# Kernel optimization log

Measured on AMD Instinct MI355X. Metric: run time of the kernel, lower is better.

## Reference

```python
import jax, jax.numpy as jnp
import numpy as np

N = 50000
E = 800000
EPS = 1e-5


def graph_conv(x, src, dst, ew, W_rel, b_rel, W_root):
    # PyG GraphConv (aggr='add'): lin_rel(sum_j e_ij * x_j) + lin_root(x_i)
    msg = x[src] * ew[:, None]                      # [E, F_in]
    agg = jax.ops.segment_sum(msg, dst, num_segments=N)  # [N, F_in]
    return agg @ W_rel.T + b_rel + x @ W_root.T


def batchnorm_relu(h, gamma, beta):
    mu = jnp.mean(h, axis=0)
    var = jnp.mean(jnp.square(h - mu), axis=0)
    hn = (h - mu) * jax.lax.rsqrt(var + EPS)
    return jax.nn.relu(hn * gamma + beta)


def setup_inputs() -> dict:
    key = jax.random.key(0)
    ks = jax.random.split(key, 16)
    d_in, h, d_out = 128, 256, 64

    def lin(k, fo, fi):
        return jax.random.normal(k, (fo, fi), jnp.float32) * (1.0 / np.sqrt(fi))

    return {
        "x": jax.random.normal(ks[0], (N, d_in), jnp.float32),
        "edge_index": jax.random.randint(ks[1], (2, E), 0, N, jnp.int32),
        "edge_weight": jax.random.uniform(ks[2], (E,), jnp.float32),
        "Wr0": lin(ks[3], h, d_in), "br0": jnp.zeros((h,), jnp.float32), "Wt0": lin(ks[4], h, d_in),
        "g0": jnp.ones((h,), jnp.float32), "be0": jnp.zeros((h,), jnp.float32),
        "Wr1": lin(ks[5], h, h), "br1": jnp.zeros((h,), jnp.float32), "Wt1": lin(ks[6], h, h),
        "g1": jnp.ones((h,), jnp.float32), "be1": jnp.zeros((h,), jnp.float32),
        "Wr2": lin(ks[7], d_out, h), "br2": jnp.zeros((d_out,), jnp.float32), "Wt2": lin(ks[8], d_out, h),
    }


def reference(x, edge_index, edge_weight, Wr0, br0, Wt0, g0, be0,
              Wr1, br1, Wt1, g1, be1, Wr2, br2, Wt2):
    src, dst = edge_index[0], edge_index[1]
    h = graph_conv(x, src, dst, edge_weight, Wr0, br0, Wt0)
    h = batchnorm_relu(h, g0, be0)
    h = graph_conv(h, src, dst, edge_weight, Wr1, br1, Wt1)
    h = batchnorm_relu(h, g1, be1)
    return graph_conv(h, src, dst, edge_weight, Wr2, br2, Wt2)
```

## Files before the change

kernel.cpp:

```cpp
#include <hip/hip_runtime.h>
#include <cstddef>
#include <cstdint>

#define SCAN_B 512

using bf16x8 = __attribute__((ext_vector_type(8))) short;
using f32x4  = __attribute__((ext_vector_type(4))) float;

__device__ __forceinline__ unsigned short f2bf(float f) {
    unsigned int u = __builtin_bit_cast(unsigned int, f);
    return (unsigned short)((u + 0x7FFFu + ((u >> 16) & 1u)) >> 16);
}
__device__ __forceinline__ float bf2f(unsigned short b) {
    unsigned int u = ((unsigned int)b) << 16;
    return __builtin_bit_cast(float, u);
}
__device__ __forceinline__ float i2f(int i) { return __builtin_bit_cast(float, i); }
__device__ __forceinline__ float u2f(unsigned int u) { return __builtin_bit_cast(float, u); }
__device__ __forceinline__ void gload_lds16(const void* g, void* l) {
    __builtin_amdgcn_global_load_lds((const __attribute__((address_space(1))) void*)g,
                                     (__attribute__((address_space(3))) void*)l, 16, 0, 0);
}

__global__ void hist_conv_k(const int* __restrict__ dst, int* __restrict__ counts,
                            int* __restrict__ rank, int E, int histBlocks,
                            const float* __restrict__ x, const float* __restrict__ Wr0,
                            const float* __restrict__ Wt0, const float* __restrict__ Wr1,
                            const float* __restrict__ Wt1, const float* __restrict__ Wr2,
                            const float* __restrict__ Wt2, unsigned short* __restrict__ x_bf,
                            unsigned short* __restrict__ Wr0b, unsigned short* __restrict__ Wt0b,
                            unsigned short* __restrict__ Wr1b, unsigned short* __restrict__ Wt1b,
                            unsigned short* __restrict__ Wr2b, unsigned short* __restrict__ Wt2b,
                            int n4x) {
    if ((int)blockIdx.x < histBlocks) {
        int e = blockIdx.x * 256 + threadIdx.x;
        if (e < E) rank[e] = atomicAdd(&counts[dst[e]], 1);
        return;
    }
    int j = (blockIdx.x - histBlocks) * 256 + threadIdx.x;
    const float* s;
    unsigned short* d;
    if (j < n4x) { s = x; d = x_bf; }
    else {
        j -= n4x;
        if (j < 8192) { s = Wr0; d = Wr0b; }
        else { j -= 8192;
        if (j < 8192) { s = Wt0; d = Wt0b; }
        else { j -= 8192;
        if (j < 16384) { s = Wr1; d = Wr1b; }
        else { j -= 16384;
        if (j < 16384) { s = Wt1; d = Wt1b; }
        else { j -= 16384;
        if (j < 4096) { s = Wr2; d = Wr2b; }
        else { j -= 4096;
        if (j >= 4096) return;
        s = Wt2; d = Wt2b; } } } } }
    }
    float4 v = reinterpret_cast<const float4*>(s)[j];
    ushort4 o;
    o.x = f2bf(v.x); o.y = f2bf(v.y); o.z = f2bf(v.z); o.w = f2bf(v.w);
    reinterpret_cast<ushort4*>(d)[j] = o;
}

__global__ void scan1_k(const int* __restrict__ counts, int* __restrict__ partial,
                        int* __restrict__ blocksum, int Nn) {
    __shared__ int sh[SCAN_B];
    int i = blockIdx.x * SCAN_B + threadIdx.x;
    int v = (i < Nn) ? counts[i] : 0;
    sh[threadIdx.x] = v;
    __syncthreads();
    for (int off = 1; off < SCAN_B; off <<= 1) {
        int t = (threadIdx.x >= (unsigned)off) ? sh[threadIdx.x - off] : 0;
        __syncthreads();
        sh[threadIdx.x] += t;
        __syncthreads();
    }
    if (i < Nn) partial[i] = sh[threadIdx.x];
    if (threadIdx.x == SCAN_B - 1) blocksum[blockIdx.x] = sh[threadIdx.x];
}

__global__ void scan3b_k(const int* __restrict__ partial, const int* __restrict__ blocksum,
                         int* __restrict__ offsets, int Nn) {
    __shared__ int add_s;
    int bx = blockIdx.x;
    if (threadIdx.x < 64) {
        int s = 0;
        for (int j = threadIdx.x; j < bx; j += 64) s += blocksum[j];
        #pragma unroll
        for (int off = 32; off > 0; off >>= 1) s += __shfl_down(s, off, 64);
        if (threadIdx.x == 0) add_s = s;
    }
    __syncthreads();
    int i = bx * SCAN_B + threadIdx.x;
    if (i >= Nn) return;
    offsets[i + 1] = partial[i] + add_s;
    if (i == 0) offsets[0] = 0;
}

__global__ void fill2_k(const int* __restrict__ src, const int* __restrict__ dst,
                        const float* __restrict__ ew, const int* __restrict__ offsets,
                        const int* __restrict__ rank, int2* __restrict__ e_sw, int E) {
    int e = blockIdx.x * blockDim.x + threadIdx.x;
    if (e >= E) return;
    int pos = offsets[dst[e]] + rank[e];
    e_sw[pos] = make_int2(src[e], __builtin_bit_cast(int, ew[e]));
}

__global__ void gather128_k(const unsigned short* __restrict__ x, const int* __restrict__ offsets,
                            const int2* __restrict__ e_sw, unsigned short* __restrict__ agg, int Nn) {
    int wid = __builtin_amdgcn_readfirstlane((blockIdx.x * blockDim.x + threadIdx.x) >> 6);
    int lane = threadIdx.x & 63;
    if (wid >= Nn) return;
    int p = offsets[wid], end = offsets[wid + 1];
    const char* xb = (const char*)x;
    const unsigned loff = lane * 4u;
    float a0 = 0.f, a1 = 0.f;
    for (; p + 8 <= end; p += 8) {
        int2 ee[8];
        #pragma unroll
        for (int i = 0; i < 8; ++i) ee[i] = e_sw[p + i];
        unsigned vv[8];
        #pragma unroll
        for (int i = 0; i < 8; ++i)
            vv[i] = *reinterpret_cast<const unsigned*>(xb + ((unsigned)ee[i].x * 256u + loff));
        #pragma unroll
        for (int i = 0; i < 8; ++i) {
            float w = i2f(ee[i].y);
            a0 += w * u2f(vv[i] << 16); a1 += w * u2f(vv[i] & 0xFFFF0000u);
        }
    }
    for (; p < end; ++p) {
        int2 e0 = e_sw[p];
        unsigned v0 = *reinterpret_cast<const unsigned*>(xb + ((unsigned)e0.x * 256u + loff));
        float w = i2f(e0.y);
        a0 += w * u2f(v0 << 16); a1 += w * u2f(v0 & 0xFFFF0000u);
    }
    unsigned o = (unsigned)f2bf(a0) | ((unsigned)f2bf(a1) << 16);
    *reinterpret_cast<unsigned*>(agg + (size_t)wid * 128 + lane * 2) = o;
}

__global__ void gather_bn_k(const unsigned short* __restrict__ h_raw,
                            const float* __restrict__ sums, const float* __restrict__ sumsq,
                            const float* __restrict__ g, const float* __restrict__ be,
                            const int* __restrict__ offsets, const int2* __restrict__ e_sw,
                            unsigned short* __restrict__ agg, unsigned short* __restrict__ hN,
                            float invN, int Nn, int gBlocks) {
    const int lane = threadIdx.x & 63;
    if ((int)blockIdx.x >= gBlocks) {
        int total4 = Nn * 64;
        int stride = (gridDim.x - gBlocks) * 256;
        for (int t = (blockIdx.x - gBlocks) * 256 + threadIdx.x; t < total4; t += stride) {
            int f0 = (t & 63) * 4;
            float4 sm = *reinterpret_cast<const float4*>(sums + f0);
            float4 sq = *reinterpret_cast<const float4*>(sumsq + f0);
            float4 gg = *reinterpret_cast<const float4*>(g + f0);
            float4 bb = *reinterpret_cast<const float4*>(be + f0);
            float smv[4] = {sm.x, sm.y, sm.z, sm.w};
            float sqv[4] = {sq.x, sq.y, sq.z, sq.w};
            float ggv[4] = {gg.x, gg.y, gg.z, gg.w};
            float bbv[4] = {bb.x, bb.y, bb.z, bb.w};
            ushort4 v = reinterpret_cast<const ushort4*>(h_raw)[t];
            unsigned short vv[4] = {v.x, v.y, v.z, v.w};
            ushort4 o;
            unsigned short* op = &o.x;
            #pragma unroll
            for (int c = 0; c < 4; ++c) {
                float mu = smv[c] * invN;
                float var = sqv[c] * invN - mu * mu;
                float sc = ggv[c] * rsqrtf(var + 1e-5f);
                float sh = bbv[c] - mu * sc;
                op[c] = f2bf(fmaxf(bf2f(vv[c]) * sc + sh, 0.f));
            }
            reinterpret_cast<ushort4*>(hN)[t] = o;
        }
        return;
    }
    int wid = __builtin_amdgcn_readfirstlane((blockIdx.x * blockDim.x + threadIdx.x) >> 6);
    if (wid >= Nn) return;
    int f0 = lane * 4;
    float4 sm = *reinterpret_cast<const float4*>(sums + f0);
    float4 sq = *reinterpret_cast<const float4*>(sumsq + f0);
    float4 gg = *reinterpret_cast<const float4*>(g + f0);
    float4 bb = *reinterpret_cast<const float4*>(be + f0);
    float sc0, sc1, sc2, sc3, sh0, sh1, sh2, sh3;
    {
        float mu, var;
        mu = sm.x * invN; var = sq.x * invN - mu * mu; sc0 = gg.x * rsqrtf(var + 1e-5f); sh0 = bb.x - mu * sc0;
        mu = sm.y * invN; var = sq.y * invN - mu * mu; sc1 = gg.y * rsqrtf(var + 1e-5f); sh1 = bb.y - mu * sc1;
        mu = sm.z * invN; var = sq.z * invN - mu * mu; sc2 = gg.z * rsqrtf(var + 1e-5f); sh2 = bb.z - mu * sc2;
        mu = sm.w * invN; var = sq.w * invN - mu * mu; sc3 = gg.w * rsqrtf(var + 1e-5f); sh3 = bb.w - mu * sc3;
    }
    int p = offsets[wid], end = offsets[wid + 1];
    const char* xb = (const char*)h_raw;
    const unsigned loff = lane * 8u;
    float a0 = 0.f, a1 = 0.f, a2 = 0.f, a3 = 0.f;
    for (; p + 8 <= end; p += 8) {
        int2 ee[8];
        #pragma unroll
        for (int i = 0; i < 8; ++i) ee[i] = e_sw[p + i];
        uint2 vv[8];
        #pragma unroll
        for (int i = 0; i < 8; ++i)
            vv[i] = *reinterpret_cast<const uint2*>(xb + ((unsigned)ee[i].x * 512u + loff));
        #pragma unroll
        for (int i = 0; i < 8; ++i) {
            float w = i2f(ee[i].y);
            a0 += w * fmaxf(u2f(vv[i].x << 16) * sc0 + sh0, 0.f);
            a1 += w * fmaxf(u2f(vv[i].x & 0xFFFF0000u) * sc1 + sh1, 0.f);
            a2 += w * fmaxf(u2f(vv[i].y << 16) * sc2 + sh2, 0.f);
            a3 += w * fmaxf(u2f(vv[i].y & 0xFFFF0000u) * sc3 + sh3, 0.f);
        }
    }
    for (; p < end; ++p) {
        int2 e0 = e_sw[p];
        uint2 v0 = *reinterpret_cast<const uint2*>(xb + ((unsigned)e0.x * 512u + loff));
        float w = i2f(e0.y);
        a0 += w * fmaxf(u2f(v0.x << 16) * sc0 + sh0, 0.f);
        a1 += w * fmaxf(u2f(v0.x & 0xFFFF0000u) * sc1 + sh1, 0.f);
        a2 += w * fmaxf(u2f(v0.y << 16) * sc2 + sh2, 0.f);
        a3 += w * fmaxf(u2f(v0.y & 0xFFFF0000u) * sc3 + sh3, 0.f);
    }
    uint2 o;
    o.x = (unsigned)f2bf(a0) | ((unsigned)f2bf(a1) << 16);
    o.y = (unsigned)f2bf(a2) | ((unsigned)f2bf(a3) << 16);
    *reinterpret_cast<uint2*>(agg + (size_t)wid * 256 + lane * 4) = o;
}

__global__ void gather_out_k(const unsigned short* __restrict__ t, const float* __restrict__ root,
                             const int* __restrict__ offsets, const int2* __restrict__ e_sw,
                             float* __restrict__ out, int Nn) {
    int gt = blockIdx.x * blockDim.x + threadIdx.x;
    int node = gt >> 4;
    int li = gt & 15;
    if (node >= Nn) return;
    int p = offsets[node], end = offsets[node + 1];
    const char* tb = (const char*)t;
    const unsigned loff = li * 8u;
    float a0 = 0.f, a1 = 0.f, a2 = 0.f, a3 = 0.f;
    for (; p + 8 <= end; p += 8) {
        int2 ee[8];
        #pragma unroll
        for (int i = 0; i < 8; ++i) ee[i] = e_sw[p + i];
        uint2 vv[8];
        #pragma unroll
        for (int i = 0; i < 8; ++i)
            vv[i] = *reinterpret_cast<const uint2*>(tb + ((unsigned)ee[i].x * 128u + loff));
        #pragma unroll
        for (int i = 0; i < 8; ++i) {
            float w = i2f(ee[i].y);
            a0 += w * u2f(vv[i].x << 16); a1 += w * u2f(vv[i].x & 0xFFFF0000u);
            a2 += w * u2f(vv[i].y << 16); a3 += w * u2f(vv[i].y & 0xFFFF0000u);
        }
    }
    for (; p < end; ++p) {
        int2 e0 = e_sw[p];
        uint2 v0 = *reinterpret_cast<const uint2*>(tb + ((unsigned)e0.x * 128u + loff));
        float w = i2f(e0.y);
        a0 += w * u2f(v0.x << 16); a1 += w * u2f(v0.x & 0xFFFF0000u);
        a2 += w * u2f(v0.y << 16); a3 += w * u2f(v0.y & 0xFFFF0000u);
    }
    float4 r = *reinterpret_cast<const float4*>(root + (size_t)node * 64 + li * 4);
    float4 o = make_float4(r.x + a0, r.y + a1, r.z + a2, r.w + a3);
    *reinterpret_cast<float4*>(out + (size_t)node * 64 + li * 4) = o;
}

template<int K, int O, int MODE>
__global__ __launch_bounds__(512, 4) void gemm_mfma_k(
        const unsigned short* __restrict__ A, const unsigned short* __restrict__ Wa,
        const unsigned short* __restrict__ X, const unsigned short* __restrict__ Wb,
        const float* __restrict__ bias, unsigned short* __restrict__ out_bf,
        float* __restrict__ out_f, float* __restrict__ sums, float* __restrict__ sumsq,
        int Nn) {
    constexpr int BM = 128, BN = 128;
    constexpr int MI = 4;
    constexpr int OJ = 2;
    constexpr int KSTEPS = K / 32;
    constexpr int NT = (MODE == 0 ? 2 : 1) * KSTEPS;
    __shared__ unsigned short As[2][BM * 32];
    __shared__ unsigned short Bs[2][BN * 32];
    const int tid = threadIdx.x;
    const int w = tid >> 6, l = tid & 63;
    const int wr = w >> 2, wc = w & 3;
    const int lrow = l & 15, kgrp = l >> 4;
    int bx = blockIdx.x;
    bx = (bx & 7) * (gridDim.x >> 3) + (bx >> 3);
    const int m0 = bx * BM;
    const int n0 = blockIdx.y * BN;
    const int srow = tid >> 2, sslot = tid & 3;
    const int gslot = sslot ^ ((srow >> 1) & 3);

    auto stage = [&](int buf, int t) {
        int ph = t / KSTEPS;
        int k0 = (t % KSTEPS) * 32;
        const unsigned short* Ap = (MODE == 0 && ph) ? X : A;
        const unsigned short* Wp = (MODE == 0 && ph) ? Wb : Wa;
        gload_lds16(Ap + (size_t)(m0 + srow) * K + k0 + (gslot << 3), &As[buf][w * 512]);
        gload_lds16(Wp + (size_t)(n0 + srow) * K + k0 + (gslot << 3), &Bs[buf][w * 512]);
    };

    f32x4 acc[MI][OJ];
    #pragma unroll
    for (int i = 0; i < MI; ++i)
        #pragma unroll
        for (int j = 0; j < OJ; ++j) {
            f32x4 z = {0.f, 0.f, 0.f, 0.f};
            acc[i][j] = z;
        }

    stage(0, 0);
    __syncthreads();
    #pragma unroll
    for (int t = 0; t < NT; ++t) {
        const int cur = t & 1;
        if (t + 1 < NT) stage(cur ^ 1, t + 1);
        bf16x8 a[MI], b[OJ];
        #pragma unroll
        for (int mi = 0; mi < MI; ++mi) {
            int row = wr * 64 + mi * 16 + lrow;
            int slot = kgrp ^ ((row >> 1) & 3);
            a[mi] = *reinterpret_cast<const bf16x8*>(&As[cur][row * 32 + slot * 8]);
        }
        #pragma unroll
        for (int oj = 0; oj < OJ; ++oj) {
            int row = wc * 32 + oj * 16 + lrow;
            int slot = kgrp ^ ((row >> 1) & 3);
            b[oj] = *reinterpret_cast<const bf16x8*>(&Bs[cur][row * 32 + slot * 8]);
        }
        #pragma unroll
        for (int mi = 0; mi < MI; ++mi)
            #pragma unroll
            for (int oj = 0; oj < OJ; ++oj)
                acc[mi][oj] = __builtin_amdgcn_mfma_f32_16x16x32_bf16(
                    a[mi], b[oj], acc[mi][oj], 0, 0, 0);
        __syncthreads();
    }

    if constexpr (MODE == 0) {
        #pragma unroll
        for (int oj = 0; oj < OJ; ++oj) {
            int col = n0 + wc * 32 + oj * 16 + lrow;
            float bcol = bias[col];
            float s = 0.f, q = 0.f;
            #pragma unroll
            for (int mi = 0; mi < MI; ++mi) {
                #pragma unroll
                for (int r = 0; r < 4; ++r) {
                    int row = m0 + wr * 64 + mi * 16 + kgrp * 4 + r;
                    float v = acc[mi][oj][r] + bcol;
                    if (row < Nn) {
                        out_bf[(size_t)row * O + col] = f2bf(v);
                        s += v; q += v * v;
                    }
                }
            }
            s += __shfl_xor(s, 16, 64); q += __shfl_xor(q, 16, 64);
            s += __shfl_xor(s, 32, 64); q += __shfl_xor(q, 32, 64);
            if (kgrp == 0) {
                atomicAdd(&sums[col], s);
                atomicAdd(&sumsq[col], q);
            }
        }
    } else {
        #pragma unroll
        for (int oj = 0; oj < OJ; ++oj) {
            int col = n0 + wc * 32 + oj * 16 + lrow;
            #pragma unroll
            for (int mi = 0; mi < MI; ++mi) {
                #pragma unroll
                for (int r = 0; r < 4; ++r) {
                    int row = m0 + wr * 64 + mi * 16 + kgrp * 4 + r;
                    if (row < Nn) {
                        if (col < 64)
                            out_bf[(size_t)row * 64 + col] = f2bf(acc[mi][oj][r]);
                        else
                            out_f[(size_t)row * 64 + (col - 64)] = acc[mi][oj][r] + bias[col - 64];
                    }
                }
            }
        }
    }
}

__global__ void bn_relu_bf_k(const unsigned short* __restrict__ h, const float* __restrict__ sums,
                             const float* __restrict__ sumsq, const float* __restrict__ g,
                             const float* __restrict__ be, unsigned short* __restrict__ hb,
                             float invN, int total4) {
    int t = blockIdx.x * blockDim.x + threadIdx.x;
    if (t >= total4) return;
    int f0 = (t & 63) * 4;
    float4 sm = *reinterpret_cast<const float4*>(sums + f0);
    float4 sq = *reinterpret_cast<const float4*>(sumsq + f0);
    float4 gg = *reinterpret_cast<const float4*>(g + f0);
    float4 bb = *reinterpret_cast<const float4*>(be + f0);
    float smv[4] = {sm.x, sm.y, sm.z, sm.w};
    float sqv[4] = {sq.x, sq.y, sq.z, sq.w};
    float ggv[4] = {gg.x, gg.y, gg.z, gg.w};
    float bbv[4] = {bb.x, bb.y, bb.z, bb.w};
    ushort4 v = reinterpret_cast<const ushort4*>(h)[t];
    unsigned short vv[4] = {v.x, v.y, v.z, v.w};
    ushort4 o;
    unsigned short* op = &o.x;
    #pragma unroll
    for (int c = 0; c < 4; ++c) {
        float mu = smv[c] * invN;
        float var = sqv[c] * invN - mu * mu;
        float sc = ggv[c] * rsqrtf(var + 1e-5f);
        float sh = bbv[c] - mu * sc;
        op[c] = f2bf(fmaxf(bf2f(vv[c]) * sc + sh, 0.f));
    }
    reinterpret_cast<ushort4*>(hb)[t] = o;
}

extern "C" void kernel_launch(void* const* d_in, const int* in_sizes, int n_in,
                              void* d_out, int out_size, void* d_ws, size_t ws_size,
                              hipStream_t stream) {
    const float* x   = (const float*)d_in[0];
    const int*   ei  = (const int*)d_in[1];
    const float* ew  = (const float*)d_in[2];
    const float* Wr0 = (const float*)d_in[3];
    const float* br0 = (const float*)d_in[4];
    const float* Wt0 = (const float*)d_in[5];
    const float* g0  = (const float*)d_in[6];
    const float* be0 = (const float*)d_in[7];
    const float* Wr1 = (const float*)d_in[8];
    const float* br1 = (const float*)d_in[9];
    const float* Wt1 = (const float*)d_in[10];
    const float* g1  = (const float*)d_in[11];
    const float* be1 = (const float*)d_in[12];
    const float* Wr2 = (const float*)d_in[13];
    const float* br2 = (const float*)d_in[14];
    const float* Wt2 = (const float*)d_in[15];

    const int E  = in_sizes[2];
    const int Nn = in_sizes[0] / 128;
    const size_t NP = 50176;
    const int* src = ei;
    const int* dst = ei + E;

    unsigned short* x_bf   = (unsigned short*)d_ws;
    unsigned short* agg_bf = x_bf + NP * 128;
    unsigned short* h0N    = agg_bf + NP * 256;
    unsigned short* h1N    = h0N + NP * 256;
    unsigned short* h_bf   = h1N + NP * 256;
    unsigned short* t_bf   = h_bf + NP * 256;
    unsigned short* wbf    = t_bf + NP * 64;
    unsigned short* Wr0b = wbf;
    unsigned short* Wt0b = wbf + 32768;
    unsigned short* Wr1b = wbf + 65536;
    unsigned short* Wt1b = wbf + 131072;
    unsigned short* W2cat = wbf + 196608;
    float* root  = (float*)(wbf + 229376);
    int2*  e_sw  = (int2*)(root + NP * 64);
    float* stats = (float*)(e_sw + E);
    int*   counts  = (int*)(stats + 4096);
    int*   partial = counts + Nn;
    int*   blocksum = partial + Nn;
    int*   rank    = blocksum + 512;
    int*   offsets = rank + E;

    dim3 blk(256);
    const int nbScan = (Nn + SCAN_B - 1) / SCAN_B;
    const float invN = 1.0f / (float)Nn;
    const int n4x = Nn * 32;
    const int histBlocks = (E + 255) / 256;
    const int convBlocks = (n4x + 57344 + 255) / 256;

    hipMemsetAsync(stats, 0, (4096 + (size_t)Nn) * sizeof(float), stream);

    hist_conv_k<<<dim3(histBlocks + convBlocks), blk, 0, stream>>>(
        dst, counts, rank, E, histBlocks,
        x, Wr0, Wt0, Wr1, Wt1, Wr2, Wt2,
        x_bf, Wr0b, Wt0b, Wr1b, Wt1b, W2cat, W2cat + 16384, n4x);
    scan1_k<<<dim3(nbScan), dim3(SCAN_B), 0, stream>>>(counts, partial, blocksum, Nn);
    scan3b_k<<<dim3(nbScan), dim3(SCAN_B), 0, stream>>>(partial, blocksum, offsets, Nn);
    fill2_k<<<dim3(histBlocks), blk, 0, stream>>>(src, dst, ew, offsets, rank, e_sw, E);

    const int gatherBlocks = (Nn * 64 + 255) / 256;

    gather128_k<<<dim3(gatherBlocks), blk, 0, stream>>>(x_bf, offsets, e_sw, agg_bf, Nn);
    gemm_mfma_k<128, 256, 0><<<dim3(NP / 128, 2), dim3(512), 0, stream>>>(
        agg_bf, Wr0b, x_bf, Wt0b, br0, h_bf, nullptr, stats + 0, stats + 256, Nn);

    gather_bn_k<<<dim3(gatherBlocks + 2048), blk, 0, stream>>>(
        h_bf, stats + 0, stats + 256, g0, be0, offsets, e_sw,
        agg_bf, h0N, invN, Nn, gatherBlocks);

    gemm_mfma_k<256, 256, 0><<<dim3(NP / 128, 2), dim3(512), 0, stream>>>(
        agg_bf, Wr1b, h0N, Wt1b, br1, h_bf, nullptr, stats + 1024, stats + 1280, Nn);
    bn_relu_bf_k<<<dim3((Nn * 64 + 255) / 256), blk, 0, stream>>>(
        h_bf, stats + 1024, stats + 1280, g1, be1, h1N, invN, Nn * 64);

    gemm_mfma_k<256, 128, 1><<<dim3(NP / 128, 1), dim3(512), 0, stream>>>(
        h1N, W2cat, nullptr, nullptr, br2, t_bf, root, nullptr, nullptr, Nn);
    gather_out_k<<<dim3((Nn * 16 + 255) / 256), blk, 0, stream>>>(
        t_bf, root, offsets, e_sw, (float*)d_out, Nn);
}
```

Measured before the change: 295.9 us.

## Fuse second BatchNorm+ReLU into final GEMM operand load

Drops the standalone BN+ReLU pass over the second hidden layer. A tiny kernel now precomputes per-feature scale and shift, and a new GEMM kernel applies scale/shift/ReLU to the A tile in registers before writing it to LDS. This saves one full read and write of the N×256 bf16 activation and one launch. In exchange, the A operand now goes through registers instead of a direct global-to-LDS load, which adds VALU work inside the GEMM main loop.

```diff
diff --git a/kernel.cpp b/kernel.cpp
--- a/kernel.cpp
+++ b/kernel.cpp
@@ -335,80 +335,147 @@
         __syncthreads();
     }
 
-    if constexpr (MODE == 0) {
-        #pragma unroll
-        for (int oj = 0; oj < OJ; ++oj) {
-            int col = n0 + wc * 32 + oj * 16 + lrow;
-            float bcol = bias[col];
-            float s = 0.f, q = 0.f;
+    #pragma unroll
+    for (int oj = 0; oj < OJ; ++oj) {
+        int col = n0 + wc * 32 + oj * 16 + lrow;
+        float bcol = bias[col];
+        float s = 0.f, q = 0.f;
+        #pragma unroll
+        for (int mi = 0; mi < MI; ++mi) {
             #pragma unroll
-            for (int mi = 0; mi < MI; ++mi) {
-                #pragma unroll
-                for (int r = 0; r < 4; ++r) {
-                    int row = m0 + wr * 64 + mi * 16 + kgrp * 4 + r;
-                    float v = acc[mi][oj][r] + bcol;
-                    if (row < Nn) {
-                        out_bf[(size_t)row * O + col] = f2bf(v);
-                        s += v; q += v * v;
-                    }
+            for (int r = 0; r < 4; ++r) {
+                int row = m0 + wr * 64 + mi * 16 + kgrp * 4 + r;
+                float v = acc[mi][oj][r] + bcol;
+                if (row < Nn) {
+                    out_bf[(size_t)row * O + col] = f2bf(v);
+                    s += v; q += v * v;
                 }
             }
-            s += __shfl_xor(s, 16, 64); q += __shfl_xor(q, 16, 64);
-            s += __shfl_xor(s, 32, 64); q += __shfl_xor(q, 32, 64);
-            if (kgrp == 0) {
-                atomicAdd(&sums[col], s);
-                atomicAdd(&sumsq[col], q);
-            }
-        }
-    } else {
+        }
+        s += __shfl_xor(s, 16, 64); q += __shfl_xor(q, 16, 64);
+        s += __shfl_xor(s, 32, 64); q += __shfl_xor(q, 32, 64);
+        if (kgrp == 0) {
+            atomicAdd(&sums[col], s);
+            atomicAdd(&sumsq[col], q);
+        }
+    }
+}
+
+__global__ void bn_coef_k(const float* __restrict__ sums, const float* __restrict__ sumsq,
+                          const float* __restrict__ g, const float* __restrict__ be,
+                          float* __restrict__ scale, float* __restrict__ shift, float invN) {
+    int f = threadIdx.x;
+    float mu = sums[f] * invN;
+    float var = sumsq[f] * invN - mu * mu;
+    float sc = g[f] * rsqrtf(var + 1e-5f);
+    scale[f] = sc;
+    shift[f] = be[f] - mu * sc;
+}
+
+template<int K>
+__global__ __launch_bounds__(512, 4) void gemm2_bn_k(
+        const unsigned short* __restrict__ A, const unsigned short* __restrict__ Wa,
+        const float* __restrict__ scale, const float* __restrict__ shift,
+        const float* __restrict__ bias, unsigned short* __restrict__ t_bf,
+        float* __restrict__ root, int Nn) {
+    constexpr int BM = 128, BN = 128;
+    constexpr int MI = 4, OJ = 2;
+    constexpr int NT = K / 32;
+    __shared__ unsigned short As[2][BM * 32];
+    __shared__ unsigned short Bs[2][BN * 32];
+    const int tid = threadIdx.x;
+    const int w = tid >> 6, l = tid & 63;
+    const int wr = w >> 2, wc = w & 3;
+    const int lrow = l & 15, kgrp = l >> 4;
+    int bx = blockIdx.x;
+    bx = (bx & 7) * (gridDim.x >> 3) + (bx >> 3);
+    const int m0 = bx * BM;
+    const int srow = tid >> 2, sslot = tid & 3;
+    const int gslot = sslot ^ ((srow >> 1) & 3);
+
+    auto stageW = [&](int buf, int t) {
+        gload_lds16(Wa + (size_t)srow * K + t * 32 + (gslot << 3), &Bs[buf][w * 512]);
+    };
+    auto loadA = [&](int t) -> bf16x8 {
+        return *reinterpret_cast<const bf16x8*>(A + (size_t)(m0 + srow) * K + t * 32 + (gslot << 3));
+    };
+    auto writeA = [&](int buf, int t, bf16x8 raw) {
+        int f0 = t * 32 + (gslot << 3);
+        float4 s0 = *reinterpret_cast<const float4*>(scale + f0);
+        float4 s1 = *reinterpret_cast<const float4*>(scale + f0 + 4);
+        float4 h0 = *reinterpret_cast<const float4*>(shift + f0);
+        float4 h1 = *reinterpret_cast<const float4*>(shift + f0 + 4);
+        float sc[8] = {s0.x, s0.y, s0.z, s0.w, s1.x, s1.y, s1.z, s1.w};
+        float sh[8] = {h0.x, h0.y, h0.z, h0.w, h1.x, h1.y, h1.z, h1.w};
+        bf16x8 o;
+        #pragma unroll
+        for (int j = 0; j < 8; ++j) {
+            float v = bf2f((unsigned short)raw[j]) * sc[j] + sh[j];
+            o[j] = (short)f2bf(fmaxf(v, 0.f));
+        }
+        *reinterpret_cast<bf16x8*>(&As[buf][tid * 8]) = o;
+    };
+
+    f32x4 acc[MI][OJ];
+    #pragma unroll
+    for (int i = 0; i < MI; ++i)
+        #pragma unroll
+        for (int j = 0; j < OJ; ++j) {
+            f32x4 z = {0.f, 0.f, 0.f, 0.f};
+            acc[i][j] = z;
+        }
+
+    {
+        bf16x8 r0 = loadA(0);
+        stageW(0, 0);
+        writeA(0, 0, r0);
+    }
+    __syncthreads();
+    #pragma unroll
+    for (int t = 0; t < NT; ++t) {
+        const int cur = t & 1;
+        bf16x8 nxt;
+        if (t + 1 < NT) { nxt = loadA(t + 1); stageW(cur ^ 1, t + 1); }
+        bf16x8 a[MI], b[OJ];
+        #pragma unroll
+        for (int mi = 0; mi < MI; ++mi) {
+            int row = wr * 64 + mi * 16 + lrow;
+            int slot = kgrp ^ ((row >> 1) & 3);
+            a[mi] = *reinterpret_cast<const bf16x8*>(&As[cur][row * 32 + slot * 8]);
+        }
         #pragma unroll
         for (int oj = 0; oj < OJ; ++oj) {
-            int col = n0 + wc * 32 + oj * 16 + lrow;
+            int row = wc * 32 + oj * 16 + lrow;
+            int slot = kgrp ^ ((row >> 1) & 3);
+            b[oj] = *reinterpret_cast<const bf16x8*>(&Bs[cur][row * 32 + slot * 8]);
+        }
+        #pragma unroll
+        for (int mi = 0; mi < MI; ++mi)
             #pragma unroll
-            for (int mi = 0; mi < MI; ++mi) {
-                #pragma unroll
-                for (int r = 0; r < 4; ++r) {
-                    int row = m0 + wr * 64 + mi * 16 + kgrp * 4 + r;
-                    if (row < Nn) {
-                        if (col < 64)
-                            out_bf[(size_t)row * 64 + col] = f2bf(acc[mi][oj][r]);
-                        else
-                            out_f[(size_t)row * 64 + (col - 64)] = acc[mi][oj][r] + bias[col - 64];
-                    }
+            for (int oj = 0; oj < OJ; ++oj)
+                acc[mi][oj] = __builtin_amdgcn_mfma_f32_16x16x32_bf16(
+                    a[mi], b[oj], acc[mi][oj], 0, 0, 0);
+        if (t + 1 < NT) writeA(cur ^ 1, t + 1, nxt);
+        __syncthreads();
+    }
+
+    #pragma unroll
+    for (int oj = 0; oj < OJ; ++oj) {
+        int col = wc * 32 + oj * 16 + lrow;
+        #pragma unroll
+        for (int mi = 0; mi < MI; ++mi) {
+            #pragma unroll
+            for (int r = 0; r < 4; ++r) {
+                int row = m0 + wr * 64 + mi * 16 + kgrp * 4 + r;
+                if (row < Nn) {
+                    if (col < 64)
+                        t_bf[(size_t)row * 64 + col] = f2bf(acc[mi][oj][r]);
+                    else
+                        root[(size_t)row * 64 + (col - 64)] = acc[mi][oj][r] + bias[col - 64];
                 }
             }
         }
     }
-}
-
-__global__ void bn_relu_bf_k(const unsigned short* __restrict__ h, const float* __restrict__ sums,
-                             const float* __restrict__ sumsq, const float* __restrict__ g,
-                             const float* __restrict__ be, unsigned short* __restrict__ hb,
-                             float invN, int total4) {
-    int t = blockIdx.x * blockDim.x + threadIdx.x;
-    if (t >= total4) return;
-    int f0 = (t & 63) * 4;
-    float4 sm = *reinterpret_cast<const float4*>(sums + f0);
-    float4 sq = *reinterpret_cast<const float4*>(sumsq + f0);
-    float4 gg = *reinterpret_cast<const float4*>(g + f0);
-    float4 bb = *reinterpret_cast<const float4*>(be + f0);
-    float smv[4] = {sm.x, sm.y, sm.z, sm.w};
-    float sqv[4] = {sq.x, sq.y, sq.z, sq.w};
-    float ggv[4] = {gg.x, gg.y, gg.z, gg.w};
-    float bbv[4] = {bb.x, bb.y, bb.z, bb.w};
-    ushort4 v = reinterpret_cast<const ushort4*>(h)[t];
-    unsigned short vv[4] = {v.x, v.y, v.z, v.w};
-    ushort4 o;
-    unsigned short* op = &o.x;
-    #pragma unroll
-    for (int c = 0; c < 4; ++c) {
-        float mu = smv[c] * invN;
-        float var = sqv[c] * invN - mu * mu;
-        float sc = ggv[c] * rsqrtf(var + 1e-5f);
-        float sh = bbv[c] - mu * sc;
-        op[c] = f2bf(fmaxf(bf2f(vv[c]) * sc + sh, 0.f));
-    }
-    reinterpret_cast<ushort4*>(hb)[t] = o;
 }
 
 extern "C" void kernel_launch(void* const* d_in, const int* in_sizes, int n_in,
@@ -487,11 +554,11 @@
 
     gemm_mfma_k<256, 256, 0><<<dim3(NP / 128, 2), dim3(512), 0, stream>>>(
         agg_bf, Wr1b, h0N, Wt1b, br1, h_bf, nullptr, stats + 1024, stats + 1280, Nn);
-    bn_relu_bf_k<<<dim3((Nn * 64 + 255) / 256), blk, 0, stream>>>(
-        h_bf, stats + 1024, stats + 1280, g1, be1, h1N, invN, Nn * 64);
-
-    gemm_mfma_k<256, 128, 1><<<dim3(NP / 128, 1), dim3(512), 0, stream>>>(
-        h1N, W2cat, nullptr, nullptr, br2, t_bf, root, nullptr, nullptr, Nn);
+
+    bn_coef_k<<<dim3(1), blk, 0, stream>>>(stats + 1024, stats + 1280, g1, be1,
+                                           stats + 1536, stats + 1792, invN);
+    gemm2_bn_k<256><<<dim3(NP / 128, 1), dim3(512), 0, stream>>>(
+        h_bf, W2cat, stats + 1536, stats + 1792, br2, t_bf, root, Nn);
     gather_out_k<<<dim3((Nn * 16 + 255) / 256), blk, 0, stream>>>(
         t_bf, root, offsets, e_sw, (float*)d_out, Nn);
 }
```

Result: faster. 289.8 us (-2.0%).
